# Performance work log

Hardware: AMD Instinct MI355X
Metric: run time of the kernel (lower is better)

The kernel has to match this reference:

```python
import jax, jax.numpy as jnp
import numpy as np

B, S, H = 512, 14, 128  # batch, encoder seq_len (hardcoded 14 in source), hidden
IN = 1                  # input_size must be 1 (see decoder permute trick)


def lstm_scan(seq, h0, c0, Wih, Whh, b):
    """seq: [T, B, in]. Returns (all_h [T,B,H], h_T, c_T). torch gate order i,f,g,o."""
    def step(carry, x_t):
        h, c = carry
        g = x_t @ Wih + h @ Whh + b              # [B, 4H]
        i, f, gg, o = jnp.split(g, 4, axis=-1)
        c = jax.nn.sigmoid(f) * c + jax.nn.sigmoid(i) * jnp.tanh(gg)
        h = jax.nn.sigmoid(o) * jnp.tanh(c)
        return (h, c), h
    (h, c), hs = jax.lax.scan(step, (h0, c0), seq)
    return hs, h, c


def setup_inputs() -> dict:
    key = jax.random.key(0)
    ks = jax.random.split(key, 12)
    s = 1.0 / np.sqrt(H)
    return {
        "inputs": jax.random.normal(ks[0], (B, S, IN), dtype=jnp.float32),
        "target_len": 8,
        "Wih_e": jax.random.normal(ks[1], (IN, 4 * H), dtype=jnp.float32) * s,
        "Whh_e": jax.random.normal(ks[2], (H, 4 * H), dtype=jnp.float32) * s,
        "b_e":   jax.random.normal(ks[3], (4 * H,), dtype=jnp.float32) * s,
        "Wih_d": jax.random.normal(ks[4], (IN, 4 * H), dtype=jnp.float32) * s,
        "Whh_d": jax.random.normal(ks[5], (H, 4 * H), dtype=jnp.float32) * s,
        "b_d":   jax.random.normal(ks[6], (4 * H,), dtype=jnp.float32) * s,
        "We": jax.random.normal(ks[7], (H, H), dtype=jnp.float32) * s,
        "Wd": jax.random.normal(ks[8], (H, H), dtype=jnp.float32) * s,
        "Wv": jax.random.normal(ks[9], (H, 1), dtype=jnp.float32) * s,
        "Wf": jax.random.normal(ks[10], (H, IN), dtype=jnp.float32) * s,
        "bf": jax.random.normal(ks[11], (IN,), dtype=jnp.float32) * s,
    }


def reference(inputs, target_len, Wih_e, Whh_e, b_e, Wih_d, Whh_d, b_d, We, Wd, Wv, Wf, bf):
    bs = inputs.shape[0]
    h0 = jnp.zeros((bs, H), inputs.dtype)
    c0 = jnp.zeros((bs, H), inputs.dtype)

    # Encoder: LSTM over the S=14 timesteps.
    hs, h_enc, c_enc = lstm_scan(inputs.transpose(1, 0, 2), h0, c0, Wih_e, Whh_e, b_e)
    enc_out = hs.transpose(1, 0, 2)  # [B, S, H]

    def dec_step(carry, _):
        x, h, c = carry  # x: [B, 1]
        # Bahdanau additive attention (recomputes enc projection each step, as in source).
        e = jnp.tanh(enc_out @ We + (h @ Wd)[:, None, :])   # [B, S, H]
        attn = jax.nn.softmax(e @ Wv, axis=1)               # [B, S, 1]
        context = jnp.sum(attn * enc_out, axis=1)           # [B, H]
        # new_input = cat(context, x) then permute -> sequence of H+1 scalars.
        seq = jnp.concatenate([context, x], axis=1).T[:, :, None]  # [H+1, B, 1]
        _, h, c = lstm_scan(seq, h, c, Wih_d, Whh_d, b_d)
        out = h @ Wf + bf  # output[:, -1, :] == final hidden -> fin_linear, [B, 1]
        return (out, h, c), (out, attn)

    (_, _, _), (outs, attns) = jax.lax.scan(
        dec_step, (inputs[:, -1, :], h_enc, c_enc), None, length=target_len)
    outputs = outs.transpose(1, 0, 2)      # [B, target_len, 1]
    total_attn = jnp.sum(attns, axis=0)    # [B, S, 1]
    return outputs, total_attn
```

## Files before the change

kernel.cpp:

```cpp
#include <hip/hip_runtime.h>

#define HDIM 128
#define SEQ  14
#define G4   512
#define TLEN 8
#define NTHR 256
#define HPITCH 160

typedef _Float16 half8 __attribute__((ext_vector_type(8)));
typedef float f32x4 __attribute__((ext_vector_type(4)));
typedef float f32x2 __attribute__((ext_vector_type(2)));

#define LOG2E  1.44269504f
#define LOG2E2 2.88539008f

__device__ __forceinline__ float frcp_(float x) { return __builtin_amdgcn_rcpf(x); }
#if defined(__has_builtin)
#if __has_builtin(__builtin_amdgcn_exp2f)
#define EXP2_(x) __builtin_amdgcn_exp2f(x)
#endif
#endif
#ifndef EXP2_
#define EXP2_(x) __expf((x) * 0.69314718f)
#endif
__device__ __forceinline__ float fsigP_(float y)  { return frcp_(1.0f + EXP2_(-y)); }
__device__ __forceinline__ float ftanhP_(float y) { return 1.0f - 2.0f * frcp_(EXP2_(y) + 1.0f); }
__device__ __forceinline__ float ftanh_(float x)  { return ftanhP_(x * LOG2E2); }

struct __align__(16) SMem {
    __align__(16) float zq[4];
    _Float16 h2[2][2][HPITCH];
    _Float16 ench[SEQ][2][HPITCH];
    _Float16 encWe[SEQ][2][HDIM];
    _Float16 hWdh[2][HDIM];
    __align__(16) float ctx2[HDIM + 1][2];
    __align__(16) float inp2[SEQ][2];
    float attnw[2][SEQ];
    float asum[2][SEQ];
    float score[2][SEQ];
    float wv[HDIM];
    float wf[HDIM];
};

__device__ __forceinline__ f32x2 lstm_core2(
    const _Float16* __restrict__ srcBase,
    _Float16* __restrict__ dstA,
    _Float16* __restrict__ dstB,
    f32x2 xv, f32x4 zeroq,
    const half8 (&whh)[4][2][4], const float (&wih)[4][2], const float (&bia)[4][2],
    float& cA, float& cB, int q, int l)
{
    const _Float16* sp = srcBase + ((l >> 2) & 1) * HPITCH + 8 * q;
    half8 a0 = *(const half8*)(sp);
    half8 a1 = *(const half8*)(sp + 32);
    half8 a2 = *(const half8*)(sp + 64);
    half8 a3 = *(const half8*)(sp + 96);
    f32x4 A[4][2];
    #pragma unroll
    for (int g = 0; g < 4; ++g) {
        #pragma unroll
        for (int tl = 0; tl < 2; ++tl) {
            f32x4 acc = __builtin_amdgcn_mfma_f32_16x16x32_f16(a0, whh[g][tl][0], zeroq, 0, 0, 0);
            acc = __builtin_amdgcn_mfma_f32_16x16x32_f16(a1, whh[g][tl][1], acc, 0, 0, 0);
            acc = __builtin_amdgcn_mfma_f32_16x16x32_f16(a2, whh[g][tl][2], acc, 0, 0, 0);
            acc = __builtin_amdgcn_mfma_f32_16x16x32_f16(a3, whh[g][tl][3], acc, 0, 0, 0);
            A[g][tl] = acc;
        }
    }
    f32x2 hn; hn[0] = 0.0f; hn[1] = 0.0f;
    if (q < 2) {
        float x = (q & 1) ? xv[1] : xv[0];
        {
            float ig = fsigP_(fmaf(x, wih[0][0], bia[0][0]) + A[0][0][0]);
            float fg = fsigP_(fmaf(x, wih[1][0], bia[1][0]) + A[1][0][0]);
            float gv = ftanhP_(fmaf(x, wih[2][0], bia[2][0]) + A[2][0][0]);
            float og = fsigP_(fmaf(x, wih[3][0], bia[3][0]) + A[3][0][0]);
            cA = fmaf(fg, cA, ig * gv);
            hn[0] = og * ftanhP_(cA * LOG2E2);
            *dstA = (_Float16)hn[0];
        }
        {
            float ig = fsigP_(fmaf(x, wih[0][1], bia[0][1]) + A[0][1][0]);
            float fg = fsigP_(fmaf(x, wih[1][1], bia[1][1]) + A[1][1][0]);
            float gv = ftanhP_(fmaf(x, wih[2][1], bia[2][1]) + A[2][1][0]);
            float og = fsigP_(fmaf(x, wih[3][1], bia[3][1]) + A[3][1][0]);
            cB = fmaf(fg, cB, ig * gv);
            hn[1] = og * ftanhP_(cB * LOG2E2);
            *dstB = (_Float16)hn[1];
        }
    }
    return hn;
}

__global__ __launch_bounds__(NTHR, 1) void seq2seq_kernel(
    const float* __restrict__ inputs,
    const float* __restrict__ Wih_e, const float* __restrict__ Whh_e, const float* __restrict__ b_e,
    const float* __restrict__ Wih_d, const float* __restrict__ Whh_d, const float* __restrict__ b_d,
    const float* __restrict__ We, const float* __restrict__ Wd,
    const float* __restrict__ Wv, const float* __restrict__ Wf, const float* __restrict__ bfp,
    float* __restrict__ out, int B)
{
    const int tid  = threadIdx.x;
    const int b0   = blockIdx.x * 2;
    const int w    = tid >> 6;
    const int lane = tid & 63;
    const int q    = lane >> 4;
    const int l    = lane & 15;
    const int colA = 32 * w + l;
    const int colB = colA + 16;
    __shared__ SMem S;

    const _Float16* s0 = &S.h2[0][0][0];
    const _Float16* s1 = &S.h2[1][0][0];
    _Float16* d0A = &S.h2[0][q & 1][colA];
    _Float16* d0B = &S.h2[0][q & 1][colB];
    _Float16* d1A = &S.h2[1][q & 1][colA];
    _Float16* d1B = &S.h2[1][q & 1][colB];

    const float gscale[4] = {LOG2E, LOG2E, LOG2E2, LOG2E};

    if (tid < 4) S.zq[tid] = 0.0f;
    if (tid < 2 * HDIM) {
        int e = tid >> 7, j = tid & 127;
        S.h2[0][e][j] = (_Float16)0.0f;
        S.h2[1][e][j] = (_Float16)0.0f;
    }
    if (tid < SEQ * 2) {
        int t = tid >> 1, m = tid & 1;
        S.inp2[t][m] = inputs[(b0 + m) * SEQ + t];
        S.asum[m][t] = 0.0f;
    }
    if (tid < HDIM) { S.wv[tid] = Wv[tid]; S.wf[tid] = Wf[tid]; }
    if (tid < 2) S.ctx2[HDIM][tid] = inputs[(b0 + tid) * SEQ + (SEQ - 1)];

    half8 whh[4][2][4];
    float wih[4][2], bia[4][2];
    #pragma unroll
    for (int g = 0; g < 4; ++g) {
        float sc = gscale[g];
        #pragma unroll
        for (int tl = 0; tl < 2; ++tl) {
            int n = g * HDIM + colA + 16 * tl;
            wih[g][tl] = Wih_e[n] * sc;
            bia[g][tl] = b_e[n] * sc;
            #pragma unroll
            for (int kt = 0; kt < 4; ++kt) {
                half8 f;
                #pragma unroll
                for (int jj = 0; jj < 8; ++jj)
                    f[jj] = (_Float16)(Whh_e[(32 * kt + 8 * q + jj) * G4 + n] * sc);
                whh[g][tl][kt] = f;
            }
        }
    }
    float cA = 0.0f, cB = 0.0f;
    __syncthreads();

    const f32x4 zeroq = *(const f32x4*)S.zq;

    f32x2 xv = *(const f32x2*)&S.inp2[0][0];
    for (int t = 0; t < SEQ; t += 2) {
        f32x2 hn = lstm_core2(s0, d1A, d1B, xv, zeroq, whh, wih, bia, cA, cB, q, l);
        if (q < 2) {
            S.ench[t][q][colA] = (_Float16)hn[0];
            S.ench[t][q][colB] = (_Float16)hn[1];
        }
        xv = *(const f32x2*)&S.inp2[t + 1][0];
        __syncthreads();
        hn = lstm_core2(s1, d0A, d0B, xv, zeroq, whh, wih, bia, cA, cB, q, l);
        if (q < 2) {
            S.ench[t + 1][q][colA] = (_Float16)hn[0];
            S.ench[t + 1][q][colB] = (_Float16)hn[1];
        }
        if (t + 2 < SEQ) xv = *(const f32x2*)&S.inp2[t + 2][0];
        __syncthreads();
    }

    {
        half8 wef[2][4];
        #pragma unroll
        for (int tl = 0; tl < 2; ++tl)
            #pragma unroll
            for (int kt = 0; kt < 4; ++kt) {
                half8 f;
                #pragma unroll
                for (int jj = 0; jj < 8; ++jj)
                    f[jj] = (_Float16)We[(32 * kt + 8 * q + jj) * HDIM + colA + 16 * tl];
                wef[tl][kt] = f;
            }
        for (int t = 0; t < SEQ; ++t) {
            const _Float16* er = &S.ench[t][0][0] + ((l >> 2) & 1) * HPITCH + 8 * q;
            half8 e0 = *(const half8*)(er);
            half8 e1 = *(const half8*)(er + 32);
            half8 e2 = *(const half8*)(er + 64);
            half8 e3 = *(const half8*)(er + 96);
            #pragma unroll
            for (int tl = 0; tl < 2; ++tl) {
                f32x4 dv = __builtin_amdgcn_mfma_f32_16x16x32_f16(e0, wef[tl][0], zeroq, 0, 0, 0);
                dv = __builtin_amdgcn_mfma_f32_16x16x32_f16(e1, wef[tl][1], dv, 0, 0, 0);
                dv = __builtin_amdgcn_mfma_f32_16x16x32_f16(e2, wef[tl][2], dv, 0, 0, 0);
                dv = __builtin_amdgcn_mfma_f32_16x16x32_f16(e3, wef[tl][3], dv, 0, 0, 0);
                if (q < 2) S.encWe[t][q][colA + 16 * tl] = (_Float16)dv[0];
            }
        }
    }

    half8 wdf[2][4];
    #pragma unroll
    for (int g = 0; g < 4; ++g) {
        float sc = gscale[g];
        #pragma unroll
        for (int tl = 0; tl < 2; ++tl) {
            int n = g * HDIM + colA + 16 * tl;
            wih[g][tl] = Wih_d[n] * sc;
            bia[g][tl] = b_d[n] * sc;
            #pragma unroll
            for (int kt = 0; kt < 4; ++kt) {
                half8 f;
                #pragma unroll
                for (int jj = 0; jj < 8; ++jj)
                    f[jj] = (_Float16)(Whh_d[(32 * kt + 8 * q + jj) * G4 + n] * sc);
                whh[g][tl][kt] = f;
            }
        }
    }
    #pragma unroll
    for (int tl = 0; tl < 2; ++tl)
        #pragma unroll
        for (int kt = 0; kt < 4; ++kt) {
            half8 f;
            #pragma unroll
            for (int jj = 0; jj < 8; ++jj)
                f[jj] = (_Float16)Wd[(32 * kt + 8 * q + jj) * HDIM + colA + 16 * tl];
            wdf[tl][kt] = f;
        }
    float bf0 = bfp[0];
    __syncthreads();

    #pragma unroll 1
    for (int dd = 0; dd < TLEN; ++dd) {
        const bool even = (dd & 1) == 0;
        const _Float16* sC = even ? s0 : s1;
        const _Float16* sO = even ? s1 : s0;
        _Float16* dCA = even ? d0A : d1A;
        _Float16* dCB = even ? d0B : d1B;
        _Float16* dOA = even ? d1A : d0A;
        _Float16* dOB = even ? d1B : d0B;

        {
            const _Float16* sp = sC + ((l >> 2) & 1) * HPITCH + 8 * q;
            half8 a0 = *(const half8*)(sp);
            half8 a1 = *(const half8*)(sp + 32);
            half8 a2 = *(const half8*)(sp + 64);
            half8 a3 = *(const half8*)(sp + 96);
            #pragma unroll
            for (int tl = 0; tl < 2; ++tl) {
                f32x4 dv = __builtin_amdgcn_mfma_f32_16x16x32_f16(a0, wdf[tl][0], zeroq, 0, 0, 0);
                dv = __builtin_amdgcn_mfma_f32_16x16x32_f16(a1, wdf[tl][1], dv, 0, 0, 0);
                dv = __builtin_amdgcn_mfma_f32_16x16x32_f16(a2, wdf[tl][2], dv, 0, 0, 0);
                dv = __builtin_amdgcn_mfma_f32_16x16x32_f16(a3, wdf[tl][3], dv, 0, 0, 0);
                if (q < 2) S.hWdh[q][colA + 16 * tl] = (_Float16)dv[0];
            }
        }
        __syncthreads();
        if (tid < 2 * SEQ * 8) {
            int p = tid >> 3, sub = tid & 7;
            int m = p & 1, t = p >> 1;
            float s = 0.0f;
            #pragma unroll
            for (int i = 0; i < 16; ++i) {
                int j = sub * 16 + i;
                s = fmaf(ftanh_((float)S.encWe[t][m][j] + (float)S.hWdh[m][j]), S.wv[j], s);
            }
            s += __shfl_down(s, 4, 8);
            s += __shfl_down(s, 2, 8);
            s += __shfl_down(s, 1, 8);
            if (sub == 0) S.score[m][t] = s;
        }
        __syncthreads();
        if (tid < 2) {
            int m = tid;
            float sc[SEQ]; float mx = -1e30f;
            #pragma unroll
            for (int t = 0; t < SEQ; ++t) { sc[t] = S.score[m][t]; mx = fmaxf(mx, sc[t]); }
            float ssum = 0.0f;
            #pragma unroll
            for (int t = 0; t < SEQ; ++t) { float e = __expf(sc[t] - mx); sc[t] = e; ssum += e; }
            float inv = frcp_(ssum);
            #pragma unroll
            for (int t = 0; t < SEQ; ++t) {
                float a = sc[t] * inv;
                S.attnw[m][t] = a;
                S.asum[m][t] += a;
            }
        }
        __syncthreads();
        {
            int e = tid >> 7, j = tid & 127;
            float a = 0.0f;
            #pragma unroll
            for (int t = 0; t < SEQ; ++t)
                a = fmaf(S.attnw[e][t], (float)S.ench[t][e][j], a);
            S.ctx2[j][e] = a;
        }
        __syncthreads();

        const f32x2* xp = (const f32x2*)&S.ctx2[0][0];
        f32x2 xd = xp[0];
        #pragma unroll 1
        for (int s2 = 0; s2 < 64; ++s2) {
            (void)lstm_core2(sC, dOA, dOB, xd, zeroq, whh, wih, bia, cA, cB, q, l);
            xd = xp[2 * s2 + 1];
            __syncthreads();
            (void)lstm_core2(sO, dCA, dCB, xd, zeroq, whh, wih, bia, cA, cB, q, l);
            xd = xp[2 * s2 + 2];
            __syncthreads();
        }
        (void)lstm_core2(sC, dOA, dOB, xd, zeroq, whh, wih, bia, cA, cB, q, l);
        __syncthreads();
        const _Float16* hO = even ? &S.h2[1][0][0] : &S.h2[0][0][0];
        if (tid < 32) {
            int m = tid >> 4, part = tid & 15;
            half8 hv = *(const half8*)(hO + m * HPITCH + part * 8);
            float s = 0.0f;
            #pragma unroll
            for (int i = 0; i < 8; ++i) s = fmaf((float)hv[i], S.wf[part * 8 + i], s);
            s += __shfl_down(s, 8, 16);
            s += __shfl_down(s, 4, 16);
            s += __shfl_down(s, 2, 16);
            s += __shfl_down(s, 1, 16);
            if (part == 0) {
                float o = s + bf0;
                out[(b0 + m) * TLEN + dd] = o;
                S.ctx2[HDIM][m] = o;
            }
        }
        __syncthreads();
    }

    if (tid < 2 * SEQ) {
        int m = tid / SEQ, t = tid % SEQ;
        out[B * TLEN + (b0 + m) * SEQ + t] = S.asum[m][t];
    }
}

extern "C" void kernel_launch(void* const* d_in, const int* in_sizes, int n_in,
                              void* d_out, int out_size, void* d_ws, size_t ws_size,
                              hipStream_t stream) {
    const float* inputs = (const float*)d_in[0];
    const float* Wih_e = (const float*)d_in[2];
    const float* Whh_e = (const float*)d_in[3];
    const float* b_e   = (const float*)d_in[4];
    const float* Wih_d = (const float*)d_in[5];
    const float* Whh_d = (const float*)d_in[6];
    const float* b_d   = (const float*)d_in[7];
    const float* We    = (const float*)d_in[8];
    const float* Wd    = (const float*)d_in[9];
    const float* Wv    = (const float*)d_in[10];
    const float* Wf    = (const float*)d_in[11];
    const float* bfp   = (const float*)d_in[12];
    float* out = (float*)d_out;

    const int B = in_sizes[0] / SEQ;

    seq2seq_kernel<<<dim3(B / 2), dim3(NTHR), 0, stream>>>(
        inputs, Wih_e, Whh_e, b_e, Wih_d, Whh_d, b_d, We, Wd, Wv, Wf, bfp, out, B);
}
```

Baseline: 623.8 us.

## Pack two independent batch pairs per workgroup with 512 threads

Each workgroup now runs 512 threads, split into two independent 256-thread halves, and each half handles its own pair of batch elements with a separate shared-memory region. The grid shrinks to B/4 blocks. Each block now has 8 waves, which may help hide the latency of the serial LSTM chain. The cost is that both halves share every __syncthreads barrier, so one half can stall the other, and with 128 blocks fewer CUs are in use.

```diff
diff --git a/kernel.cpp b/kernel.cpp
--- a/kernel.cpp
+++ b/kernel.cpp
@@ -4,7 +4,7 @@
 #define SEQ  14
 #define G4   512
 #define TLEN 8
-#define NTHR 256
+#define NTHR 512
 #define HPITCH 160
 
 typedef _Float16 half8 __attribute__((ext_vector_type(8)));
@@ -27,8 +27,7 @@
 __device__ __forceinline__ float ftanhP_(float y) { return 1.0f - 2.0f * frcp_(EXP2_(y) + 1.0f); }
 __device__ __forceinline__ float ftanh_(float x)  { return ftanhP_(x * LOG2E2); }
 
-struct __align__(16) SMem {
-    __align__(16) float zq[4];
+struct __align__(16) PairMem {
     _Float16 h2[2][2][HPITCH];
     _Float16 ench[SEQ][2][HPITCH];
     _Float16 encWe[SEQ][2][HDIM];
@@ -38,6 +37,11 @@
     float attnw[2][SEQ];
     float asum[2][SEQ];
     float score[2][SEQ];
+};
+
+struct __align__(16) SMem {
+    __align__(16) float zq[4];
+    PairMem P[2];
     float wv[HDIM];
     float wf[HDIM];
 };
@@ -101,37 +105,41 @@
     float* __restrict__ out, int B)
 {
     const int tid  = threadIdx.x;
-    const int b0   = blockIdx.x * 2;
-    const int w    = tid >> 6;
+    const int p    = tid >> 8;
+    const int t5   = tid & 255;
+    const int b0   = blockIdx.x * 4 + 2 * p;
+    const int w    = t5 >> 6;
     const int lane = tid & 63;
     const int q    = lane >> 4;
     const int l    = lane & 15;
     const int colA = 32 * w + l;
     const int colB = colA + 16;
     __shared__ SMem S;
-
-    const _Float16* s0 = &S.h2[0][0][0];
-    const _Float16* s1 = &S.h2[1][0][0];
-    _Float16* d0A = &S.h2[0][q & 1][colA];
-    _Float16* d0B = &S.h2[0][q & 1][colB];
-    _Float16* d1A = &S.h2[1][q & 1][colA];
-    _Float16* d1B = &S.h2[1][q & 1][colB];
+    PairMem* __restrict__ PP = &S.P[p];
+
+    const _Float16* s0 = &PP->h2[0][0][0];
+    const _Float16* s1 = &PP->h2[1][0][0];
+    _Float16* d0A = &PP->h2[0][q & 1][colA];
+    _Float16* d0B = &PP->h2[0][q & 1][colB];
+    _Float16* d1A = &PP->h2[1][q & 1][colA];
+    _Float16* d1B = &PP->h2[1][q & 1][colB];
 
     const float gscale[4] = {LOG2E, LOG2E, LOG2E2, LOG2E};
 
     if (tid < 4) S.zq[tid] = 0.0f;
-    if (tid < 2 * HDIM) {
-        int e = tid >> 7, j = tid & 127;
-        S.h2[0][e][j] = (_Float16)0.0f;
-        S.h2[1][e][j] = (_Float16)0.0f;
-    }
-    if (tid < SEQ * 2) {
-        int t = tid >> 1, m = tid & 1;
-        S.inp2[t][m] = inputs[(b0 + m) * SEQ + t];
-        S.asum[m][t] = 0.0f;
+    #pragma unroll
+    for (int idx = 0; idx < 2; ++idx) {
+        int r = t5 + 256 * idx;
+        int buf = r >> 8, e = (r >> 7) & 1, j = r & 127;
+        PP->h2[buf][e][j] = (_Float16)0.0f;
+    }
+    if (t5 < SEQ * 2) {
+        int t = t5 >> 1, m = t5 & 1;
+        PP->inp2[t][m] = inputs[(b0 + m) * SEQ + t];
+        PP->asum[m][t] = 0.0f;
     }
     if (tid < HDIM) { S.wv[tid] = Wv[tid]; S.wf[tid] = Wf[tid]; }
-    if (tid < 2) S.ctx2[HDIM][tid] = inputs[(b0 + tid) * SEQ + (SEQ - 1)];
+    if (t5 < 2) PP->ctx2[HDIM][t5] = inputs[(b0 + t5) * SEQ + (SEQ - 1)];
 
     half8 whh[4][2][4];
     float wih[4][2], bia[4][2];
@@ -158,21 +166,21 @@
 
     const f32x4 zeroq = *(const f32x4*)S.zq;
 
-    f32x2 xv = *(const f32x2*)&S.inp2[0][0];
+    f32x2 xv = *(const f32x2*)&PP->inp2[0][0];
     for (int t = 0; t < SEQ; t += 2) {
         f32x2 hn = lstm_core2(s0, d1A, d1B, xv, zeroq, whh, wih, bia, cA, cB, q, l);
         if (q < 2) {
-            S.ench[t][q][colA] = (_Float16)hn[0];
-            S.ench[t][q][colB] = (_Float16)hn[1];
-        }
-        xv = *(const f32x2*)&S.inp2[t + 1][0];
+            PP->ench[t][q][colA] = (_Float16)hn[0];
+            PP->ench[t][q][colB] = (_Float16)hn[1];
+        }
+        xv = *(const f32x2*)&PP->inp2[t + 1][0];
         __syncthreads();
         hn = lstm_core2(s1, d0A, d0B, xv, zeroq, whh, wih, bia, cA, cB, q, l);
         if (q < 2) {
-            S.ench[t + 1][q][colA] = (_Float16)hn[0];
-            S.ench[t + 1][q][colB] = (_Float16)hn[1];
-        }
-        if (t + 2 < SEQ) xv = *(const f32x2*)&S.inp2[t + 2][0];
+            PP->ench[t + 1][q][colA] = (_Float16)hn[0];
+            PP->ench[t + 1][q][colB] = (_Float16)hn[1];
+        }
+        if (t + 2 < SEQ) xv = *(const f32x2*)&PP->inp2[t + 2][0];
         __syncthreads();
     }
 
@@ -189,7 +197,7 @@
                 wef[tl][kt] = f;
             }
         for (int t = 0; t < SEQ; ++t) {
-            const _Float16* er = &S.ench[t][0][0] + ((l >> 2) & 1) * HPITCH + 8 * q;
+            const _Float16* er = &PP->ench[t][0][0] + ((l >> 2) & 1) * HPITCH + 8 * q;
             half8 e0 = *(const half8*)(er);
             half8 e1 = *(const half8*)(er + 32);
             half8 e2 = *(const half8*)(er + 64);
@@ -200,7 +208,7 @@
                 dv = __builtin_amdgcn_mfma_f32_16x16x32_f16(e1, wef[tl][1], dv, 0, 0, 0);
                 dv = __builtin_amdgcn_mfma_f32_16x16x32_f16(e2, wef[tl][2], dv, 0, 0, 0);
                 dv = __builtin_amdgcn_mfma_f32_16x16x32_f16(e3, wef[tl][3], dv, 0, 0, 0);
-                if (q < 2) S.encWe[t][q][colA + 16 * tl] = (_Float16)dv[0];
+                if (q < 2) PP->encWe[t][q][colA + 16 * tl] = (_Float16)dv[0];
             }
         }
     }
@@ -259,30 +267,30 @@
                 dv = __builtin_amdgcn_mfma_f32_16x16x32_f16(a1, wdf[tl][1], dv, 0, 0, 0);
                 dv = __builtin_amdgcn_mfma_f32_16x16x32_f16(a2, wdf[tl][2], dv, 0, 0, 0);
                 dv = __builtin_amdgcn_mfma_f32_16x16x32_f16(a3, wdf[tl][3], dv, 0, 0, 0);
-                if (q < 2) S.hWdh[q][colA + 16 * tl] = (_Float16)dv[0];
-            }
-        }
-        __syncthreads();
-        if (tid < 2 * SEQ * 8) {
-            int p = tid >> 3, sub = tid & 7;
-            int m = p & 1, t = p >> 1;
+                if (q < 2) PP->hWdh[q][colA + 16 * tl] = (_Float16)dv[0];
+            }
+        }
+        __syncthreads();
+        if (t5 < 2 * SEQ * 8) {
+            int pr = t5 >> 3, sub = t5 & 7;
+            int m = pr & 1, t = pr >> 1;
             float s = 0.0f;
             #pragma unroll
             for (int i = 0; i < 16; ++i) {
                 int j = sub * 16 + i;
-                s = fmaf(ftanh_((float)S.encWe[t][m][j] + (float)S.hWdh[m][j]), S.wv[j], s);
+                s = fmaf(ftanh_((float)PP->encWe[t][m][j] + (float)PP->hWdh[m][j]), S.wv[j], s);
             }
             s += __shfl_down(s, 4, 8);
             s += __shfl_down(s, 2, 8);
             s += __shfl_down(s, 1, 8);
-            if (sub == 0) S.score[m][t] = s;
-        }
-        __syncthreads();
-        if (tid < 2) {
-            int m = tid;
+            if (sub == 0) PP->score[m][t] = s;
+        }
+        __syncthreads();
+        if (t5 < 2) {
+            int m = t5;
             float sc[SEQ]; float mx = -1e30f;
             #pragma unroll
-            for (int t = 0; t < SEQ; ++t) { sc[t] = S.score[m][t]; mx = fmaxf(mx, sc[t]); }
+            for (int t = 0; t < SEQ; ++t) { sc[t] = PP->score[m][t]; mx = fmaxf(mx, sc[t]); }
             float ssum = 0.0f;
             #pragma unroll
             for (int t = 0; t < SEQ; ++t) { float e = __expf(sc[t] - mx); sc[t] = e; ssum += e; }
@@ -290,22 +298,22 @@
             #pragma unroll
             for (int t = 0; t < SEQ; ++t) {
                 float a = sc[t] * inv;
-                S.attnw[m][t] = a;
-                S.asum[m][t] += a;
+                PP->attnw[m][t] = a;
+                PP->asum[m][t] += a;
             }
         }
         __syncthreads();
         {
-            int e = tid >> 7, j = tid & 127;
+            int e = t5 >> 7, j = t5 & 127;
             float a = 0.0f;
             #pragma unroll
             for (int t = 0; t < SEQ; ++t)
-                a = fmaf(S.attnw[e][t], (float)S.ench[t][e][j], a);
-            S.ctx2[j][e] = a;
-        }
-        __syncthreads();
-
-        const f32x2* xp = (const f32x2*)&S.ctx2[0][0];
+                a = fmaf(PP->attnw[e][t], (float)PP->ench[t][e][j], a);
+            PP->ctx2[j][e] = a;
+        }
+        __syncthreads();
+
+        const f32x2* xp = (const f32x2*)&PP->ctx2[0][0];
         f32x2 xd = xp[0];
         #pragma unroll 1
         for (int s2 = 0; s2 < 64; ++s2) {
@@ -318,9 +326,9 @@
         }
         (void)lstm_core2(sC, dOA, dOB, xd, zeroq, whh, wih, bia, cA, cB, q, l);
         __syncthreads();
-        const _Float16* hO = even ? &S.h2[1][0][0] : &S.h2[0][0][0];
-        if (tid < 32) {
-            int m = tid >> 4, part = tid & 15;
+        const _Float16* hO = even ? &PP->h2[1][0][0] : &PP->h2[0][0][0];
+        if (t5 < 32) {
+            int m = t5 >> 4, part = t5 & 15;
             half8 hv = *(const half8*)(hO + m * HPITCH + part * 8);
             float s = 0.0f;
             #pragma unroll
@@ -332,15 +340,15 @@
             if (part == 0) {
                 float o = s + bf0;
                 out[(b0 + m) * TLEN + dd] = o;
-                S.ctx2[HDIM][m] = o;
-            }
-        }
-        __syncthreads();
-    }
-
-    if (tid < 2 * SEQ) {
-        int m = tid / SEQ, t = tid % SEQ;
-        out[B * TLEN + (b0 + m) * SEQ + t] = S.asum[m][t];
+                PP->ctx2[HDIM][m] = o;
+            }
+        }
+        __syncthreads();
+    }
+
+    if (t5 < 2 * SEQ) {
+        int m = t5 / SEQ, t = t5 % SEQ;
+        out[B * TLEN + (b0 + m) * SEQ + t] = PP->asum[m][t];
     }
 }
 
@@ -363,6 +371,6 @@
 
     const int B = in_sizes[0] / SEQ;
 
-    seq2seq_kernel<<<dim3(B / 2), dim3(NTHR), 0, stream>>>(
+    seq2seq_kernel<<<dim3(B / 4), dim3(NTHR), 0, stream>>>(
         inputs, Wih_e, Whh_e, b_e, Wih_d, Whh_d, b_d, We, Wd, Wv, Wf, bfp, out, B);
 }
```

New measurement: 865.0 us. +38.7%, slower.
